# Kernel tuning notes

Hardware: AMD Instinct MI355X
Metric: run time of the kernel (lower is better)

The kernel has to match this reference:

```python
import jax, jax.numpy as jnp
import numpy as np

# Structure constants (equal-sized graphs; first SPG nodes of each graph are sentence nodes)
B = 64          # graphs in batch
NPG = 1024      # nodes per graph
SPG = 64        # sentence nodes per graph
N = B * NPG     # 65536 total nodes
E = 524288      # total edges (within-graph)
C = 256         # in_channels
H = 512         # TopKPooling hardcoded hidden
KS = 3          # num_output_sentences
KO = int(np.ceil(0.5 * (NPG - SPG)))  # ratio=0.5 -> 480 'other' nodes kept per graph
SLOPE = 0.01    # LeakyReLU default negative slope


def gcn_conv(x, row, col, w, W, b, n):
    """PyG GCNConv with edge_weight: add self-loops (weight 1), symmetric norm, aggregate at col."""
    loop = jnp.arange(n, dtype=row.dtype)
    row2 = jnp.concatenate([row, loop])
    col2 = jnp.concatenate([col, loop])
    w2 = jnp.concatenate([w, jnp.ones((n,), w.dtype)])
    deg = jax.ops.segment_sum(w2, col2, num_segments=n)
    dinv = jnp.where(deg > 0, jax.lax.rsqrt(jnp.where(deg > 0, deg, 1.0)), 0.0)
    norm = dinv[row2] * w2 * dinv[col2]          # [E+N]
    h = x @ W                                     # [N, out]
    out = jax.ops.segment_sum(norm[:, None] * h[row2], col2, num_segments=n)
    return out + b


def setup_inputs() -> dict:
    key = jax.random.key(0)
    ks = jax.random.split(key, 6)
    x = jax.random.normal(ks[0], (N, C), jnp.float32)
    # within-graph random edges
    gid = jnp.arange(E, dtype=jnp.int32) // (E // B)
    src = jax.random.randint(ks[1], (E,), 0, NPG, dtype=jnp.int32) + gid * NPG
    dst = jax.random.randint(ks[2], (E,), 0, NPG, dtype=jnp.int32) + gid * NPG
    edge_index = jnp.stack([src, dst], axis=0)
    edge_attr = jax.random.uniform(ks[3], (E, 1), jnp.float32, 0.1, 1.0)
    batch = jnp.repeat(jnp.arange(B, dtype=jnp.int32), NPG)
    W1 = jax.random.normal(ks[4], (C, H), jnp.float32) * (1.0 / np.sqrt(C))
    b1 = jnp.zeros((H,), jnp.float32)
    W2 = jax.random.normal(ks[5], (H, 1), jnp.float32) * (1.0 / np.sqrt(H))
    b2 = jnp.zeros((1,), jnp.float32)
    return {"x": x, "edge_index": edge_index, "edge_attr": edge_attr, "batch": batch,
            "W1": W1, "b1": b1, "W2": W2, "b2": b2}


def reference(x, edge_index, edge_attr, batch, W1, b1, W2, b2):
    row, col = edge_index[0], edge_index[1]
    w = edge_attr[:, 0]                           # edge_weight = edge_attr.squeeze()
    # 2-layer GCN scorer
    h = gcn_conv(x, row, col, w, W1, b1, N)
    h = jnp.where(h > 0, h, SLOPE * h)            # LeakyReLU
    score = gcn_conv(h, row, col, w, W2, b2, N)[:, 0]
    score = jnp.nan_to_num(score)
    sg = score.reshape(B, NPG)                    # dense per-graph scores (graphs equal-sized)
    # per-graph top-k: 3 sentence nodes, ceil(0.5*other) other nodes
    _, si = jax.lax.top_k(sg[:, :SPG], KS)        # [B, KS] local idx among sentence nodes
    sent_perm = (si + jnp.arange(B)[:, None] * NPG).reshape(-1)
    _, oi = jax.lax.top_k(sg[:, SPG:], KO)        # [B, KO] local idx among other nodes
    other_perm = (oi + SPG + jnp.arange(B)[:, None] * NPG).reshape(-1)
    perm = jnp.concatenate([sent_perm, other_perm])  # [B*(KS+KO)]
    # gather + scale (multiplier = 1)
    score_perm = score[perm]
    x_out = x[perm] * score_perm[:, None]
    batch_out = batch[perm]
    # filter_adj (padded: dropped edges marked -1 / zeroed; 'keep' mask returned)
    mask = jnp.full((N,), -1, dtype=perm.dtype).at[perm].set(jnp.arange(perm.shape[0], dtype=perm.dtype))
    nr, nc = mask[row], mask[col]
    keep = (nr >= 0) & (nc >= 0)
    ei_new = jnp.where(keep, jnp.stack([nr, nc], axis=0), -1)
    ea_new = jnp.where(keep[:, None], edge_attr, 0.0)
    sentence_scores = sg[:, :SPG].reshape(-1)
    sentence_batch = jnp.repeat(jnp.arange(B, dtype=batch.dtype), SPG)
    return (x_out, ei_new, ea_new, batch_out, perm, score_perm, sentence_scores, sentence_batch, keep)
```

## Files before the change

### kernel.cpp

```cpp
#include <hip/hip_runtime.h>

#define NN   65536
#define NE   524288
#define EPG  8192

#define O1 7913472
#define O2 8962048
#define O3 9486336
#define O4 9517248
#define O5 9548160
#define O6 9579072
#define O7 9583168
#define O8 9587264

#define CSR_OFF    8388608
#define DINV_OFF   9437184
#define Z_OFF      9502720
#define W1HI_OFF   9568256
#define RSTART_OFF 9633792
#define CURSOR_OFF 9699344
#define W1LO_OFF   9764880
#define HIST_OFF   9830416
#define SCORE_OFF  65536
#define YLO_OFF    4194304

typedef __attribute__((ext_vector_type(8))) short bfrag;
typedef __attribute__((ext_vector_type(4))) float f32x4;
typedef __attribute__((ext_vector_type(8))) unsigned short us8;
typedef __attribute__((ext_vector_type(2))) unsigned long long u64x2;

__device__ __forceinline__ unsigned monof(float f) {
  unsigned u = __float_as_uint(f);
  return (u & 0x80000000u) ? ~u : (u | 0x80000000u);
}

__device__ __forceinline__ unsigned short bf16rne(float f) {
  unsigned u = __float_as_uint(f);
  return (unsigned short)((u + 0x7FFFu + ((u >> 16) & 1u)) >> 16);
}

__global__ void k_zero(unsigned long long* __restrict__ hist, float* __restrict__ z) {
  int n = blockIdx.x * 256 + threadIdx.x;
  if (n < NN) { hist[n] = 0ull; z[n] = 0.0f; }
}

__global__ void k_hist(const int* __restrict__ ei, const float* __restrict__ w,
                       unsigned long long* __restrict__ hist) {
  int e = blockIdx.x * 256 + threadIdx.x;
  if (e < NE) {
    int c = ei[NE + e];
    unsigned long long add = (1ull << 40) |
        (unsigned long long)(unsigned)__float2uint_rn(w[e] * 1048576.0f);
    atomicAdd(&hist[c], add);
  }
}

__global__ __launch_bounds__(256) void k_prefix(const unsigned long long* __restrict__ hist,
    unsigned* __restrict__ rstart, unsigned* __restrict__ cursor, float* __restrict__ dinv) {
  __shared__ unsigned tmp[2][256];
  int g = blockIdx.x, t = threadIdx.x;
  int base = g << 10;
  unsigned c[4], sum = 0;
  unsigned long long hv[4];
#pragma unroll
  for (int u = 0; u < 4; ++u) {
    hv[u] = hist[base + t * 4 + u];
    c[u] = (unsigned)(hv[u] >> 40);
    sum += c[u];
  }
  tmp[0][t] = sum;
  __syncthreads();
  int pin = 0;
  for (int off = 1; off < 256; off <<= 1) {
    int pout = pin ^ 1;
    unsigned v = tmp[pin][t];
    if (t >= off) v += tmp[pin][t - off];
    tmp[pout][t] = v;
    __syncthreads();
    pin = pout;
  }
  unsigned run = (t == 0) ? 0u : tmp[pin][t - 1];
#pragma unroll
  for (int u = 0; u < 4; ++u) {
    unsigned pos = (unsigned)(g << 13) + run;
    rstart[base + t * 4 + u] = pos;
    cursor[base + t * 4 + u] = pos;
    run += c[u];
  }
#pragma unroll
  for (int u = 0; u < 4; ++u) {
    int n = base + t * 4 + u;
    float wsum = 1.0f + (float)(hv[u] & ((1ull << 40) - 1)) * 9.5367431640625e-07f;
    dinv[n] = rsqrtf(wsum);
  }
  if (g == 0 && t == 0) rstart[NN] = NE;
}

__global__ __launch_bounds__(256) void k_w1t(const float* __restrict__ W1,
    unsigned short* __restrict__ hi, unsigned short* __restrict__ lo) {
  __shared__ unsigned short sh[64][72], sl[64][72];
  int bk = blockIdx.x & 3, bc = blockIdx.x >> 2;
  int k0 = bk * 64, c0 = bc * 64;
  int t = threadIdx.x;
#pragma unroll
  for (int s = 0; s < 16; ++s) {
    int i = t + s * 256;
    int k = i >> 6, c = i & 63;
    float v = W1[(k0 + k) * 512 + c0 + c];
    unsigned short h = bf16rne(v);
    float hf = __uint_as_float((unsigned)h << 16);
    sh[c][k] = h;
    sl[c][k] = bf16rne(v - hf);
  }
  __syncthreads();
#pragma unroll
  for (int s = 0; s < 16; ++s) {
    int i = t + s * 256;
    int c = i >> 6, k = i & 63;
    hi[(c0 + c) * 256 + k0 + k] = sh[c][k];
    lo[(c0 + c) * 256 + k0 + k] = sl[c][k];
  }
}

__global__ void k_scatter(const int* __restrict__ ei, const float* __restrict__ w,
                          const float* __restrict__ dinv, unsigned* __restrict__ cursor,
                          unsigned long long* __restrict__ csr) {
  int e = blockIdx.x * 256 + threadIdx.x;
  if (e < NE) {
    int r = ei[e], c = ei[NE + e];
    float cf = w[e] * dinv[r] * dinv[c];
    unsigned pos = atomicAdd(&cursor[c], 1u);
    unsigned sl = (unsigned)(r & 1023);
    csr[pos] = ((unsigned long long)__float_as_uint(cf) << 32) |
               (sl << 15) | (sl * 18u);
  }
}

__global__ __launch_bounds__(1024, 1) void k_aggx(const float* __restrict__ x,
    const unsigned long long* __restrict__ csr, const unsigned* __restrict__ rstart,
    const float* __restrict__ dinv, unsigned short* __restrict__ yhi,
    unsigned short* __restrict__ ylo, int gbase) {
  __shared__ float xs[1024 * 18];
  __shared__ unsigned long long es[8193];
  __shared__ unsigned rp[1025];
  __shared__ float dv2[1024];
  int bid = blockIdx.x;
  int g  = bid & 31;
  int cc = bid >> 5;
  int gg = gbase + g;
  int c0 = cc * 16;
  int t = threadIdx.x;
  int nbase = gg << 10;
  unsigned ebase = (unsigned)gg << 13;
  {
    rp[t] = rstart[nbase + t] - ebase;
    float dv = dinv[nbase + t];
    dv2[t] = dv * dv;
  }
  if (t == 0) { rp[1024] = 8192u; es[8192] = 0ull; }
  {
    const u64x2* src = (const u64x2*)(csr + ebase);
    u64x2* dst = (u64x2*)es;
#pragma unroll
    for (int i = 0; i < 4; ++i)
      dst[t + i * 1024] = src[t + i * 1024];
  }
#pragma unroll
  for (int s = 0; s < 4; ++s) {
    int i = t + s * 1024;
    int row = i >> 2, q = (i & 3) * 4;
    float4 v = *(const float4*)&x[(nbase + row) * 256 + c0 + q];
    float* d = &xs[row * 18 + q];
    *(float2*)&d[0] = make_float2(v.x, v.y);
    *(float2*)&d[2] = make_float2(v.z, v.w);
  }
  __syncthreads();
  int jj = t & 7;
  int h  = (t >> 3) & 1;
  int grp = t >> 4;
  int dbase = grp * 16;
  int j2 = 2 * jj;
  for (int dd = 0; dd < 8; ++dd) {
    int d0 = dbase + dd;
    unsigned pA = rp[d0], qA = rp[d0 + 1];
    unsigned pB = rp[d0 + 8], qB = rp[d0 + 9];
    int L0 = (int)(qA - pA), L1 = (int)(qB - pB);
    int L = L0 > L1 ? L0 : L1;
    int d = d0 + 8 * h;
    unsigned p = h ? pB : pA;
    unsigned q = h ? qB : qA;
    float2 xv = *(const float2*)&xs[d * 18 + j2];
    float dv = dv2[d];
    float ax = dv * xv.x, ay = dv * xv.y;
    for (int k = 0; k < L; k += 4) {
      unsigned long long cv[4];
#pragma unroll
      for (int u = 0; u < 4; ++u) {
        unsigned a = p + (unsigned)(k + u);
        cv[u] = es[a < q ? a : 8192u];
      }
#pragma unroll
      for (int u = 0; u < 4; ++u) {
        float cf = __uint_as_float((unsigned)(cv[u] >> 32));
        const float2 xr = *(const float2*)&xs[((unsigned)cv[u] & 0x7FFFu) + j2];
        ax += cf * xr.x;
        ay += cf * xr.y;
      }
    }
    int idx = ((g << 10) + d) * 256 + c0 + j2;
    unsigned short hx = bf16rne(ax), hy = bf16rne(ay);
    float lx = ax - __uint_as_float((unsigned)hx << 16);
    float ly = ay - __uint_as_float((unsigned)hy << 16);
    *(unsigned*)&yhi[idx] = (unsigned)hx | ((unsigned)hy << 16);
    *(unsigned*)&ylo[idx] = (unsigned)bf16rne(lx) | ((unsigned)bf16rne(ly) << 16);
  }
}

__global__ __launch_bounds__(256, 2) void k_gemm(
    const unsigned short* __restrict__ yhi, const unsigned short* __restrict__ ylo,
    const unsigned short* __restrict__ w1hi, const unsigned short* __restrict__ w1lo,
    const float* __restrict__ b1, const float* __restrict__ W2,
    float* __restrict__ z, int node_base) {
  __shared__ unsigned short Ah_s[128 * 40], Al_s[128 * 40];
  __shared__ unsigned short Bh_s[128 * 40], Bl_s[128 * 40];
  int bx = blockIdx.x & 3, by = blockIdx.x >> 2;
  int r0 = by * 128, c0 = bx * 128;
  int t = threadIdx.x;
  int lane = t & 63, wid = t >> 6;
  int wr = wid >> 1, wc = wid & 1;
  int lr = lane & 15, hg = lane >> 4;
  f32x4 acc[4][4];
#pragma unroll
  for (int m = 0; m < 4; ++m)
#pragma unroll
    for (int n = 0; n < 4; ++n)
      acc[m][n] = (f32x4){0.0f, 0.0f, 0.0f, 0.0f};
  int rr = t >> 2, kq = (t & 3) * 8;
  for (int kt = 0; kt < 256; kt += 32) {
    us8 va0 = *(const us8*)&yhi[(r0 + rr) * 256 + kt + kq];
    us8 va1 = *(const us8*)&yhi[(r0 + rr + 64) * 256 + kt + kq];
    us8 vb0 = *(const us8*)&ylo[(r0 + rr) * 256 + kt + kq];
    us8 vb1 = *(const us8*)&ylo[(r0 + rr + 64) * 256 + kt + kq];
    us8 vc0 = *(const us8*)&w1hi[(c0 + rr) * 256 + kt + kq];
    us8 vc1 = *(const us8*)&w1hi[(c0 + rr + 64) * 256 + kt + kq];
    us8 vd0 = *(const us8*)&w1lo[(c0 + rr) * 256 + kt + kq];
    us8 vd1 = *(const us8*)&w1lo[(c0 + rr + 64) * 256 + kt + kq];
    __syncthreads();
    *(us8*)&Ah_s[rr * 40 + kq] = va0;  *(us8*)&Ah_s[(rr + 64) * 40 + kq] = va1;
    *(us8*)&Al_s[rr * 40 + kq] = vb0;  *(us8*)&Al_s[(rr + 64) * 40 + kq] = vb1;
    *(us8*)&Bh_s[rr * 40 + kq] = vc0;  *(us8*)&Bh_s[(rr + 64) * 40 + kq] = vc1;
    *(us8*)&Bl_s[rr * 40 + kq] = vd0;  *(us8*)&Bl_s[(rr + 64) * 40 + kq] = vd1;
    __syncthreads();
    bfrag Ah[4], Al[4], Bh[4], Bl[4];
#pragma unroll
    for (int m = 0; m < 4; ++m) {
      int ra = (wr * 64 + m * 16 + lr) * 40 + hg * 8;
      Ah[m] = *(const bfrag*)&Ah_s[ra];
      Al[m] = *(const bfrag*)&Al_s[ra];
      int rb = (wc * 64 + m * 16 + lr) * 40 + hg * 8;
      Bh[m] = *(const bfrag*)&Bh_s[rb];
      Bl[m] = *(const bfrag*)&Bl_s[rb];
    }
#pragma unroll
    for (int m = 0; m < 4; ++m)
#pragma unroll
      for (int n = 0; n < 4; ++n) {
        acc[m][n] = __builtin_amdgcn_mfma_f32_16x16x32_bf16(Ah[m], Bh[n], acc[m][n], 0, 0, 0);
        acc[m][n] = __builtin_amdgcn_mfma_f32_16x16x32_bf16(Ah[m], Bl[n], acc[m][n], 0, 0, 0);
        acc[m][n] = __builtin_amdgcn_mfma_f32_16x16x32_bf16(Al[m], Bh[n], acc[m][n], 0, 0, 0);
      }
  }
  float p[4][4];
#pragma unroll
  for (int m = 0; m < 4; ++m)
#pragma unroll
    for (int i = 0; i < 4; ++i) p[m][i] = 0.0f;
#pragma unroll
  for (int n = 0; n < 4; ++n) {
    int col = c0 + wc * 64 + n * 16 + lr;
    float b1v = b1[col], w2v = W2[col];
#pragma unroll
    for (int m = 0; m < 4; ++m)
#pragma unroll
      for (int i = 0; i < 4; ++i) {
        float v = acc[m][n][i] + b1v;
        v = v > 0.0f ? v : 0.01f * v;
        p[m][i] += v * w2v;
      }
  }
#pragma unroll
  for (int off = 8; off > 0; off >>= 1)
#pragma unroll
    for (int m = 0; m < 4; ++m)
#pragma unroll
      for (int i = 0; i < 4; ++i)
        p[m][i] += __shfl_xor(p[m][i], off, 16);
  if (lr == 0) {
    int rbase = node_base + r0 + wr * 64 + hg * 4;
#pragma unroll
    for (int m = 0; m < 4; ++m)
#pragma unroll
      for (int i = 0; i < 4; ++i)
        unsafeAtomicAdd(&z[rbase + m * 16 + i], p[m][i]);
  }
}

__global__ void k_score(const unsigned long long* __restrict__ csr,
                        const unsigned* __restrict__ rstart,
                        const float* __restrict__ dinv, const float* __restrict__ z,
                        const float* __restrict__ b2, float* __restrict__ score,
                        int* __restrict__ mask) {
  int n = blockIdx.x * 256 + threadIdx.x;
  if (n >= NN) return;
  mask[n] = -1;
  int nb = n & ~1023;
  float dv = dinv[n];
  float a = b2[0] + dv * dv * z[n];
  unsigned s = rstart[n], epos = rstart[n + 1];
  for (unsigned e = s; e < epos; ++e) {
    unsigned long long p = csr[e];
    a += __uint_as_float((unsigned)(p >> 32)) * z[nb + (((unsigned)p >> 15) & 1023u)];
  }
  score[n] = a;
}

__device__ void bitonic(unsigned long long* keys, int n, int t, int nt) {
  for (int k = 2; k <= n; k <<= 1)
    for (int jj = k >> 1; jj > 0; jj >>= 1) {
      __syncthreads();
      for (int i = t; i < n; i += nt) {
        int ixj = i ^ jj;
        if (ixj > i) {
          unsigned long long a = keys[i], c = keys[ixj];
          bool up = ((i & k) == 0);
          if ((a > c) == up) { keys[i] = c; keys[ixj] = a; }
        }
      }
    }
  __syncthreads();
}

__global__ __launch_bounds__(256) void k_topk(const float* __restrict__ score,
                                              int* __restrict__ mask,
                                              float* __restrict__ out) {
  __shared__ unsigned long long keys[1024];
  int b = blockIdx.x, t = threadIdx.x;
  int base = b << 10;
  if (t < 64) {
    float v = score[base + t];
    keys[t] = ((unsigned long long)(~monof(v)) << 32) | (unsigned)t;
    out[O6 + b * 64 + t] = v;
    out[O7 + b * 64 + t] = (float)b;
  }
  __syncthreads();
  bitonic(keys, 64, t, 256);
  if (t < 3) {
    int idx = (int)(keys[t] & 0xFFFFFFFFull);
    int node = base + idx;
    int pos = b * 3 + t;
    mask[node] = pos;
    out[O4 + pos] = (float)node;
    out[O5 + pos] = score[node];
    out[O3 + pos] = (float)b;
  }
  __syncthreads();
  for (int i = t; i < 1024; i += 256) {
    if (i < 960) {
      float v = score[base + 64 + i];
      keys[i] = ((unsigned long long)(~monof(v)) << 32) | (unsigned)i;
    } else {
      keys[i] = 0xFFFFFFFFFFFFFFFFull;
    }
  }
  __syncthreads();
  bitonic(keys, 1024, t, 256);
  for (int r = t; r < 480; r += 256) {
    int idx = (int)(keys[r] & 0xFFFFFFFFull);
    int node = base + 64 + idx;
    int pos = 192 + b * 480 + r;
    mask[node] = pos;
    out[O4 + pos] = (float)node;
    out[O5 + pos] = score[node];
    out[O3 + pos] = (float)b;
  }
}

__global__ void k_edges(const int* __restrict__ ei, const float* __restrict__ w,
                        const int* __restrict__ mask, float* __restrict__ out) {
  int e = blockIdx.x * 256 + threadIdx.x;
  if (e >= NE) return;
  int nr = mask[ei[e]];
  int nc = mask[ei[NE + e]];
  bool keep = (nr >= 0) && (nc >= 0);
  out[O1 + e]      = keep ? (float)nr : -1.0f;
  out[O1 + NE + e] = keep ? (float)nc : -1.0f;
  out[O2 + e]      = keep ? w[e] : 0.0f;
  out[O8 + e]      = keep ? 1.0f : 0.0f;
}

__global__ void k_xout(const float* __restrict__ x, const float* __restrict__ permF,
                       const float* __restrict__ scoreP, float* __restrict__ out) {
  int i = blockIdx.x;
  int node = (int)permF[i];
  float s = scoreP[i];
  const float4* xr = (const float4*)&x[node * 256];
  float4* o = (float4*)&out[i * 256];
  float4 v = xr[threadIdx.x];
  o[threadIdx.x] = make_float4(v.x * s, v.y * s, v.z * s, v.w * s);
}

extern "C" void kernel_launch(void* const* d_in, const int* in_sizes, int n_in,
                              void* d_out, int out_size, void* d_ws, size_t ws_size,
                              hipStream_t stream) {
  (void)in_sizes; (void)n_in; (void)out_size; (void)d_ws; (void)ws_size;
  const float* x  = (const float*)d_in[0];
  const int*   ei = (const int*)d_in[1];
  const float* w  = (const float*)d_in[2];
  const float* W1 = (const float*)d_in[4];
  const float* b1 = (const float*)d_in[5];
  const float* W2 = (const float*)d_in[6];
  const float* b2 = (const float*)d_in[7];
  float* out    = (float*)d_out;
  unsigned short* yhi = (unsigned short*)out;
  unsigned short* ylo = (unsigned short*)(out + YLO_OFF);
  unsigned long long* csr = (unsigned long long*)(out + CSR_OFF);
  float* dinv   = out + DINV_OFF;
  float* z      = out + Z_OFF;
  unsigned* rstart = (unsigned*)(out + RSTART_OFF);
  unsigned* cursor = (unsigned*)(out + CURSOR_OFF);
  unsigned long long* hist64 = (unsigned long long*)(out + HIST_OFF);
  unsigned short* w1hi = (unsigned short*)(out + W1HI_OFF);
  unsigned short* w1lo = (unsigned short*)(out + W1LO_OFF);
  float* score  = out + SCORE_OFF;
  int*   mask   = (int*)d_out;

  k_zero<<<256, 256, 0, stream>>>(hist64, z);
  k_hist<<<2048, 256, 0, stream>>>(ei, w, hist64);
  k_prefix<<<64, 256, 0, stream>>>(hist64, rstart, cursor, dinv);
  k_w1t<<<32, 256, 0, stream>>>(W1, w1hi, w1lo);
  k_scatter<<<2048, 256, 0, stream>>>(ei, w, dinv, cursor, csr);
  for (int ch = 0; ch < 2; ++ch) {
    k_aggx<<<512, 1024, 0, stream>>>(x, csr, rstart, dinv, yhi, ylo, ch * 32);
    k_gemm<<<1024, 256, 0, stream>>>(yhi, ylo, w1hi, w1lo, b1, W2, z, ch * 32768);
  }
  k_score<<<256, 256, 0, stream>>>(csr, rstart, dinv, z, b2, score, mask);
  k_topk<<<64, 256, 0, stream>>>(score, mask, out);
  k_edges<<<2048, 256, 0, stream>>>(ei, w, mask, out);
  k_xout<<<30912, 64, 0, stream>>>(x, out + O4, out + O5, out);
}
```

Measured before the change: 251.2 us.

## Merge small kernels, load GEMM fragments directly from global, widen topk blocks

Fuses the zero and W1-transpose kernels into one launch, and the edge-filter and x-gather kernels into one tail kernel. This removes launch gaps and lets small independent work overlap. The GEMM drops its LDS staging and barriers: each wave loads its bf16 MFMA fragments straight from global memory, and occupancy rises to 3 blocks per SIMD. Top-k sorting now uses 512 threads per block. Uncoalesced fragment loads and duplicate global reads in the GEMM could raise memory traffic in exchange for fewer syncs.

```diff
diff --git a/kernel.cpp b/kernel.cpp
--- a/kernel.cpp
+++ b/kernel.cpp
@@ -26,7 +26,6 @@
 
 typedef __attribute__((ext_vector_type(8))) short bfrag;
 typedef __attribute__((ext_vector_type(4))) float f32x4;
-typedef __attribute__((ext_vector_type(8))) unsigned short us8;
 typedef __attribute__((ext_vector_type(2))) unsigned long long u64x2;
 
 __device__ __forceinline__ unsigned monof(float f) {
@@ -39,9 +38,38 @@
   return (unsigned short)((u + 0x7FFFu + ((u >> 16) & 1u)) >> 16);
 }
 
-__global__ void k_zero(unsigned long long* __restrict__ hist, float* __restrict__ z) {
-  int n = blockIdx.x * 256 + threadIdx.x;
-  if (n < NN) { hist[n] = 0ull; z[n] = 0.0f; }
+__global__ __launch_bounds__(256) void k_zero_w1t(unsigned long long* __restrict__ hist,
+    float* __restrict__ z, const float* __restrict__ W1,
+    unsigned short* __restrict__ hi, unsigned short* __restrict__ lo) {
+  __shared__ unsigned short sh[64][72], sl[64][72];
+  int b = blockIdx.x, t = threadIdx.x;
+  if (b < 256) {
+    int n = b * 256 + t;
+    hist[n] = 0ull;
+    z[n] = 0.0f;
+    return;
+  }
+  int bb = b - 256;
+  int bk = bb & 3, bc = bb >> 2;
+  int k0 = bk * 64, c0 = bc * 64;
+#pragma unroll
+  for (int s = 0; s < 16; ++s) {
+    int i = t + s * 256;
+    int k = i >> 6, c = i & 63;
+    float v = W1[(k0 + k) * 512 + c0 + c];
+    unsigned short h = bf16rne(v);
+    float hf = __uint_as_float((unsigned)h << 16);
+    sh[c][k] = h;
+    sl[c][k] = bf16rne(v - hf);
+  }
+  __syncthreads();
+#pragma unroll
+  for (int s = 0; s < 16; ++s) {
+    int i = t + s * 256;
+    int c = i >> 6, k = i & 63;
+    hi[(c0 + c) * 256 + k0 + k] = sh[c][k];
+    lo[(c0 + c) * 256 + k0 + k] = sl[c][k];
+  }
 }
 
 __global__ void k_hist(const int* __restrict__ ei, const float* __restrict__ w,
@@ -94,32 +122,6 @@
     dinv[n] = rsqrtf(wsum);
   }
   if (g == 0 && t == 0) rstart[NN] = NE;
-}
-
-__global__ __launch_bounds__(256) void k_w1t(const float* __restrict__ W1,
-    unsigned short* __restrict__ hi, unsigned short* __restrict__ lo) {
-  __shared__ unsigned short sh[64][72], sl[64][72];
-  int bk = blockIdx.x & 3, bc = blockIdx.x >> 2;
-  int k0 = bk * 64, c0 = bc * 64;
-  int t = threadIdx.x;
-#pragma unroll
-  for (int s = 0; s < 16; ++s) {
-    int i = t + s * 256;
-    int k = i >> 6, c = i & 63;
-    float v = W1[(k0 + k) * 512 + c0 + c];
-    unsigned short h = bf16rne(v);
-    float hf = __uint_as_float((unsigned)h << 16);
-    sh[c][k] = h;
-    sl[c][k] = bf16rne(v - hf);
-  }
-  __syncthreads();
-#pragma unroll
-  for (int s = 0; s < 16; ++s) {
-    int i = t + s * 256;
-    int c = i >> 6, k = i & 63;
-    hi[(c0 + c) * 256 + k0 + k] = sh[c][k];
-    lo[(c0 + c) * 256 + k0 + k] = sl[c][k];
-  }
 }
 
 __global__ void k_scatter(const int* __restrict__ ei, const float* __restrict__ w,
@@ -216,13 +218,11 @@
   }
 }
 
-__global__ __launch_bounds__(256, 2) void k_gemm(
+__global__ __launch_bounds__(256, 3) void k_gemm(
     const unsigned short* __restrict__ yhi, const unsigned short* __restrict__ ylo,
     const unsigned short* __restrict__ w1hi, const unsigned short* __restrict__ w1lo,
     const float* __restrict__ b1, const float* __restrict__ W2,
     float* __restrict__ z, int node_base) {
-  __shared__ unsigned short Ah_s[128 * 40], Al_s[128 * 40];
-  __shared__ unsigned short Bh_s[128 * 40], Bl_s[128 * 40];
   int bx = blockIdx.x & 3, by = blockIdx.x >> 2;
   int r0 = by * 128, c0 = bx * 128;
   int t = threadIdx.x;
@@ -235,31 +235,21 @@
 #pragma unroll
     for (int n = 0; n < 4; ++n)
       acc[m][n] = (f32x4){0.0f, 0.0f, 0.0f, 0.0f};
-  int rr = t >> 2, kq = (t & 3) * 8;
+  int arow[4], bcol[4];
+#pragma unroll
+  for (int m = 0; m < 4; ++m) {
+    arow[m] = (r0 + wr * 64 + m * 16 + lr) * 256 + hg * 8;
+    bcol[m] = (c0 + wc * 64 + m * 16 + lr) * 256 + hg * 8;
+  }
+#pragma unroll 2
   for (int kt = 0; kt < 256; kt += 32) {
-    us8 va0 = *(const us8*)&yhi[(r0 + rr) * 256 + kt + kq];
-    us8 va1 = *(const us8*)&yhi[(r0 + rr + 64) * 256 + kt + kq];
-    us8 vb0 = *(const us8*)&ylo[(r0 + rr) * 256 + kt + kq];
-    us8 vb1 = *(const us8*)&ylo[(r0 + rr + 64) * 256 + kt + kq];
-    us8 vc0 = *(const us8*)&w1hi[(c0 + rr) * 256 + kt + kq];
-    us8 vc1 = *(const us8*)&w1hi[(c0 + rr + 64) * 256 + kt + kq];
-    us8 vd0 = *(const us8*)&w1lo[(c0 + rr) * 256 + kt + kq];
-    us8 vd1 = *(const us8*)&w1lo[(c0 + rr + 64) * 256 + kt + kq];
-    __syncthreads();
-    *(us8*)&Ah_s[rr * 40 + kq] = va0;  *(us8*)&Ah_s[(rr + 64) * 40 + kq] = va1;
-    *(us8*)&Al_s[rr * 40 + kq] = vb0;  *(us8*)&Al_s[(rr + 64) * 40 + kq] = vb1;
-    *(us8*)&Bh_s[rr * 40 + kq] = vc0;  *(us8*)&Bh_s[(rr + 64) * 40 + kq] = vc1;
-    *(us8*)&Bl_s[rr * 40 + kq] = vd0;  *(us8*)&Bl_s[(rr + 64) * 40 + kq] = vd1;
-    __syncthreads();
     bfrag Ah[4], Al[4], Bh[4], Bl[4];
 #pragma unroll
     for (int m = 0; m < 4; ++m) {
-      int ra = (wr * 64 + m * 16 + lr) * 40 + hg * 8;
-      Ah[m] = *(const bfrag*)&Ah_s[ra];
-      Al[m] = *(const bfrag*)&Al_s[ra];
-      int rb = (wc * 64 + m * 16 + lr) * 40 + hg * 8;
-      Bh[m] = *(const bfrag*)&Bh_s[rb];
-      Bl[m] = *(const bfrag*)&Bl_s[rb];
+      Ah[m] = *(const bfrag*)&yhi[arow[m] + kt];
+      Al[m] = *(const bfrag*)&ylo[arow[m] + kt];
+      Bh[m] = *(const bfrag*)&w1hi[bcol[m] + kt];
+      Bl[m] = *(const bfrag*)&w1lo[bcol[m] + kt];
     }
 #pragma unroll
     for (int m = 0; m < 4; ++m)
@@ -340,7 +330,7 @@
   __syncthreads();
 }
 
-__global__ __launch_bounds__(256) void k_topk(const float* __restrict__ score,
+__global__ __launch_bounds__(512) void k_topk(const float* __restrict__ score,
                                               int* __restrict__ mask,
                                               float* __restrict__ out) {
   __shared__ unsigned long long keys[1024];
@@ -353,7 +343,7 @@
     out[O7 + b * 64 + t] = (float)b;
   }
   __syncthreads();
-  bitonic(keys, 64, t, 256);
+  bitonic(keys, 64, t, 512);
   if (t < 3) {
     int idx = (int)(keys[t] & 0xFFFFFFFFull);
     int node = base + idx;
@@ -364,7 +354,7 @@
     out[O3 + pos] = (float)b;
   }
   __syncthreads();
-  for (int i = t; i < 1024; i += 256) {
+  for (int i = t; i < 1024; i += 512) {
     if (i < 960) {
       float v = score[base + 64 + i];
       keys[i] = ((unsigned long long)(~monof(v)) << 32) | (unsigned)i;
@@ -373,8 +363,8 @@
     }
   }
   __syncthreads();
-  bitonic(keys, 1024, t, 256);
-  for (int r = t; r < 480; r += 256) {
+  bitonic(keys, 1024, t, 512);
+  for (int r = t; r < 480; r += 512) {
     int idx = (int)(keys[r] & 0xFFFFFFFFull);
     int node = base + 64 + idx;
     int pos = 192 + b * 480 + r;
@@ -385,28 +375,27 @@
   }
 }
 
-__global__ void k_edges(const int* __restrict__ ei, const float* __restrict__ w,
-                        const int* __restrict__ mask, float* __restrict__ out) {
-  int e = blockIdx.x * 256 + threadIdx.x;
-  if (e >= NE) return;
-  int nr = mask[ei[e]];
-  int nc = mask[ei[NE + e]];
-  bool keep = (nr >= 0) && (nc >= 0);
-  out[O1 + e]      = keep ? (float)nr : -1.0f;
-  out[O1 + NE + e] = keep ? (float)nc : -1.0f;
-  out[O2 + e]      = keep ? w[e] : 0.0f;
-  out[O8 + e]      = keep ? 1.0f : 0.0f;
-}
-
-__global__ void k_xout(const float* __restrict__ x, const float* __restrict__ permF,
-                       const float* __restrict__ scoreP, float* __restrict__ out) {
-  int i = blockIdx.x;
-  int node = (int)permF[i];
-  float s = scoreP[i];
-  const float4* xr = (const float4*)&x[node * 256];
-  float4* o = (float4*)&out[i * 256];
-  float4 v = xr[threadIdx.x];
-  o[threadIdx.x] = make_float4(v.x * s, v.y * s, v.z * s, v.w * s);
+__global__ __launch_bounds__(256) void k_tail(const int* __restrict__ ei,
+    const float* __restrict__ w, const int* __restrict__ mask,
+    const float* __restrict__ x, float* __restrict__ out) {
+  int bid = blockIdx.x, t = threadIdx.x;
+  if (bid < 2048) {
+    int e = bid * 256 + t;
+    int nr = mask[ei[e]];
+    int nc = mask[ei[NE + e]];
+    bool keep = (nr >= 0) && (nc >= 0);
+    out[O1 + e]      = keep ? (float)nr : -1.0f;
+    out[O1 + NE + e] = keep ? (float)nc : -1.0f;
+    out[O2 + e]      = keep ? w[e] : 0.0f;
+    out[O8 + e]      = keep ? 1.0f : 0.0f;
+  } else {
+    int i = (bid - 2048) * 4 + (t >> 6);
+    int lane = t & 63;
+    int node = (int)out[O4 + i];
+    float s = out[O5 + i];
+    float4 v = ((const float4*)&x[node * 256])[lane];
+    ((float4*)&out[i * 256])[lane] = make_float4(v.x * s, v.y * s, v.z * s, v.w * s);
+  }
 }
 
 extern "C" void kernel_launch(void* const* d_in, const int* in_sizes, int n_in,
@@ -434,17 +423,15 @@
   float* score  = out + SCORE_OFF;
   int*   mask   = (int*)d_out;
 
-  k_zero<<<256, 256, 0, stream>>>(hist64, z);
+  k_zero_w1t<<<288, 256, 0, stream>>>(hist64, z, W1, w1hi, w1lo);
   k_hist<<<2048, 256, 0, stream>>>(ei, w, hist64);
   k_prefix<<<64, 256, 0, stream>>>(hist64, rstart, cursor, dinv);
-  k_w1t<<<32, 256, 0, stream>>>(W1, w1hi, w1lo);
   k_scatter<<<2048, 256, 0, stream>>>(ei, w, dinv, cursor, csr);
   for (int ch = 0; ch < 2; ++ch) {
     k_aggx<<<512, 1024, 0, stream>>>(x, csr, rstart, dinv, yhi, ylo, ch * 32);
     k_gemm<<<1024, 256, 0, stream>>>(yhi, ylo, w1hi, w1lo, b1, W2, z, ch * 32768);
   }
   k_score<<<256, 256, 0, stream>>>(csr, rstart, dinv, z, b2, score, mask);
-  k_topk<<<64, 256, 0, stream>>>(score, mask, out);
-  k_edges<<<2048, 256, 0, stream>>>(ei, w, mask, out);
-  k_xout<<<30912, 64, 0, stream>>>(x, out + O4, out + O5, out);
-}
+  k_topk<<<64, 512, 0, stream>>>(score, mask, out);
+  k_tail<<<2048 + 7728, 256, 0, stream>>>(ei, w, mask, x, out);
+}
```

Result: slower. 313.0 us (+24.6%).
